# Performance work log

Hardware: AMD Instinct MI355X
Metric: run time of the kernel (lower is better)

Reference implementation:

```python
import jax, jax.numpy as jnp
import numpy as np

NUM_HEADS = 16

def setup_inputs() -> dict:
    key = jax.random.key(0)
    ks = jax.random.split(key, 5)
    B, N, C = 2, 2048, 1024
    x = jax.random.normal(ks[0], (B, N, C), dtype=jnp.float32)
    s_in = 1.0 / np.sqrt(C)
    Wq = jax.random.normal(ks[1], (C, 2 * C), dtype=jnp.float32) * s_in
    Wk = jax.random.normal(ks[2], (C, 2 * C), dtype=jnp.float32) * s_in
    Wv = jax.random.normal(ks[3], (C, 2 * C), dtype=jnp.float32) * s_in
    Wo = jax.random.normal(ks[4], (2 * C, C), dtype=jnp.float32) * (1.0 / np.sqrt(2 * C))
    return {"x": x, "Wq": Wq, "Wk": Wk, "Wv": Wv, "Wo": Wo}

def reference(x, Wq, Wk, Wv, Wo):
    B, N, C = x.shape
    H = NUM_HEADS
    hd = C // H  # head_dim
    def proj(W):
        # [B,N,2C] -> [B,H,N,2*hd]
        return (x @ W).reshape(B, N, H, 2 * hd).transpose(0, 2, 1, 3)
    q = proj(Wq)
    k = proj(Wk)
    v = proj(Wv)
    q_r, q_i = q[..., :hd], q[..., hd:]
    k_r, k_i = k[..., :hd], k[..., hd:]
    v_r, v_i = v[..., :hd], v[..., hd:]
    # complex inner product real part: Re(Q K^H) = q_r.k_r + q_i.k_i
    scores = (jnp.einsum('bhnd,bhmd->bhnm', q_r, k_r)
              + jnp.einsum('bhnd,bhmd->bhnm', q_i, k_i)) / jnp.sqrt(jnp.float32(hd))
    causal = jnp.tril(jnp.ones((N, N), dtype=bool))  # [N,N]
    scores = jnp.where(causal[None, None], scores, -jnp.inf)
    probs = jax.nn.softmax(scores, axis=-1)  # dropout off (eval mode)
    out_r = jnp.einsum('bhnm,bhmd->bhnd', probs, v_r)
    out_i = jnp.einsum('bhnm,bhmd->bhnd', probs, v_i)
    out = jnp.concatenate([out_r, out_i], axis=-1)  # [B,H,N,2*hd]
    out = out.transpose(0, 2, 1, 3).reshape(B, N, 2 * C)
    return out @ Wo  # [B,N,C]
```

## Files before the change

### kernel.cpp

```cpp
#include <hip/hip_runtime.h>
#include <hip/hip_bf16.h>
#include <stdint.h>
#include <cmath>

using bf16 = __hip_bfloat16;
typedef __attribute__((ext_vector_type(8))) short bf16x8;
typedef __attribute__((ext_vector_type(4))) short bf16x4;
typedef __attribute__((ext_vector_type(4))) float f32x4;

#define MFMA16(a, b, c) __builtin_amdgcn_mfma_f32_16x16x32_bf16(a, b, c, 0, 0, 0)

#if defined(__has_builtin)
#if __has_builtin(__builtin_amdgcn_mfma_f32_16x16x16bf16_1k)
#define HAVE_MFMA_K16 1
#endif
#if __has_builtin(__builtin_amdgcn_exp2f)
#define EXP2F __builtin_amdgcn_exp2f
#endif
#endif
#ifndef HAVE_MFMA_K16
#define HAVE_MFMA_K16 0
#endif
#ifndef EXP2F
#define EXP2F exp2f
#endif

#define NEG_BIG (-1e30f)
#define K2SCALE 0.18033688011112042f

__device__ __forceinline__ short f2bf(float v) {
  return __builtin_bit_cast(short, __float2bfloat16(v));
}

__device__ __forceinline__ f32x4 pv_mfma(bf16x4 va, bf16x4 pb, f32x4 c) {
#if HAVE_MFMA_K16
  return __builtin_amdgcn_mfma_f32_16x16x16bf16_1k(va, pb, c, 0, 0, 0);
#else
  const bf16x8 a = {va[0], va[1], va[2], va[3], 0, 0, 0, 0};
  const bf16x8 b = {pb[0], pb[1], pb[2], pb[3], 0, 0, 0, 0};
  return MFMA16(a, b, c);
#endif
}

__device__ __forceinline__ void async_ld16(const bf16* g, bf16* l) {
  __builtin_amdgcn_global_load_lds(
      (const __attribute__((address_space(1))) unsigned int*)g,
      (__attribute__((address_space(3))) unsigned int*)l, 16, 0, 0);
}

template <typename T> __device__ __forceinline__ T cvt_out(float v);
template <> __device__ __forceinline__ float cvt_out<float>(float v) { return v; }
template <> __device__ __forceinline__ bf16 cvt_out<bf16>(float v) { return __float2bfloat16(v); }

__global__ void prep(const float* __restrict__ x,
                     const float* __restrict__ Wq, const float* __restrict__ Wk,
                     const float* __restrict__ Wv, const float* __restrict__ Wo,
                     bf16* __restrict__ xb, bf16* __restrict__ tq,
                     bf16* __restrict__ tk, bf16* __restrict__ tv,
                     bf16* __restrict__ to_) {
  __shared__ bf16 tile[32][33];
  const int bid = blockIdx.x;
  if (bid < 8192) {
    const int z = bid >> 11, tt = bid & 2047;
    const float* in = z == 0 ? Wq : z == 1 ? Wk : z == 2 ? Wv : Wo;
    bf16* out = z == 0 ? tq : z == 1 ? tk : z == 2 ? tv : to_;
    int R, Cc, c0, r0;
    if (z < 3) { R = 1024; Cc = 2048; c0 = (tt & 63) * 32; r0 = (tt >> 6) * 32; }
    else       { R = 2048; Cc = 1024; c0 = (tt & 31) * 32; r0 = (tt >> 5) * 32; }
    const int xx = threadIdx.x & 31;
    const int y = threadIdx.x >> 5;
#pragma unroll
    for (int yy = y; yy < 32; yy += 8)
      tile[yy][xx] = __float2bfloat16(in[(size_t)(r0 + yy) * Cc + c0 + xx]);
    __syncthreads();
#pragma unroll
    for (int yy = y; yy < 32; yy += 8)
      out[(size_t)(c0 + yy) * R + r0 + xx] = tile[xx][yy];
  } else {
    const int i = (bid - 8192) * 256 + threadIdx.x;
    const float4 v = ((const float4*)x)[i];
    bf16 o[4] = {__float2bfloat16(v.x), __float2bfloat16(v.y),
                 __float2bfloat16(v.z), __float2bfloat16(v.w)};
    *(uint64_t*)&xb[i * 4] = *(const uint64_t*)o;
  }
}

__global__ __launch_bounds__(256)
void gemm_qkv(const bf16* __restrict__ xb, const bf16* __restrict__ wq,
              const bf16* __restrict__ wk, const bf16* __restrict__ wv,
              bf16* __restrict__ qo, bf16* __restrict__ ko, bf16* __restrict__ vo) {
  __shared__ __align__(16) bf16 As[128 * 32];
  __shared__ __align__(16) bf16 Bs[128 * 32];
  const int op = blockIdx.y;
  const int bid = blockIdx.x;
  const bf16 *A, *B;
  int m0, n0;
  if (op < 2) { A = xb; B = op ? wk : wq; m0 = (bid >> 4) * 128; n0 = (bid & 15) * 128; }
  else        { A = wv; B = xb;           m0 = (bid & 15) * 128; n0 = (bid >> 4) * 128; }
  const int K = 1024;

  const int t = threadIdx.x;
  const int l = t & 63, w = t >> 6;
  const int q4 = l >> 4, li = l & 15;
  const int wr = (w >> 1) * 64, wc = (w & 1) * 64;

  f32x4 acc[4][4] = {};
  const int colst = (t & 3) * 8;
  const bf16* gA = A + (size_t)m0 * K;
  const bf16* gB = B + (size_t)n0 * K;

  for (int k0 = 0; k0 < K; k0 += 32) {
#pragma unroll
    for (int p = 0; p < 2; ++p) {
      const int row = p * 64 + (t >> 2);
      const int lbase = p * 2048 + (t & ~63) * 8;
      async_ld16(gA + (size_t)row * K + k0 + colst, &As[lbase]);
      async_ld16(gB + (size_t)row * K + k0 + colst, &Bs[lbase]);
    }
    __syncthreads();
    bf16x8 af[4], bfr[4];
#pragma unroll
    for (int i = 0; i < 4; ++i)
      af[i] = *(const bf16x8*)&As[(wr + i * 16 + li) * 32 + q4 * 8];
#pragma unroll
    for (int j = 0; j < 4; ++j)
      bfr[j] = *(const bf16x8*)&Bs[(wc + j * 16 + li) * 32 + q4 * 8];
#pragma unroll
    for (int i = 0; i < 4; ++i)
#pragma unroll
      for (int j = 0; j < 4; ++j)
        acc[i][j] = MFMA16(af[i], bfr[j], acc[i][j]);
    __syncthreads();
  }

#pragma unroll
  for (int i = 0; i < 4; ++i)
#pragma unroll
    for (int j = 0; j < 4; ++j)
#pragma unroll
      for (int r = 0; r < 4; ++r) {
        const int gm = m0 + wr + i * 16 + q4 * 4 + r;
        const int gn = n0 + wc + j * 16 + li;
        const bf16 v = __float2bfloat16(acc[i][j][r]);
        if (op < 2) {
          const int b = gm >> 11, nn = gm & 2047;
          const int h = gn >> 7, d = gn & 127;
          (op ? ko : qo)[((size_t)(b * 16 + h) * 2048 + nn) * 128 + d] = v;
        } else {
          const int h = gm >> 7, d = gm & 127;
          const int b = gn >> 11, nn = gn & 2047;
          vo[((size_t)(b * 16 + h) * 128 + d) * 2048 + nn] = v;
        }
      }
}

template <int NT, typename OT>
__global__ __launch_bounds__(256)
void gemm_bt(const bf16* __restrict__ A, const bf16* __restrict__ B,
             OT* __restrict__ C, int M, int N, int K) {
  __shared__ __align__(16) bf16 As[128 * 32];
  __shared__ __align__(16) bf16 Bs[NT * 32];
  constexpr int JN = NT / 32;
  const int t = threadIdx.x;
  const int l = t & 63, w = t >> 6;
  const int q4 = l >> 4, li = l & 15;
  const int m0 = blockIdx.y * 128;
  const int n0 = blockIdx.x * NT;
  const int wr = (w >> 1) * 64, wc = (w & 1) * (NT / 2);

  f32x4 acc[4][JN] = {};
  const int colst = (t & 3) * 8;
  const bf16* gA = A + (size_t)m0 * K;
  const bf16* gB = B + (size_t)n0 * K;

  for (int k0 = 0; k0 < K; k0 += 32) {
#pragma unroll
    for (int p = 0; p < 2; ++p) {
      const int row = p * 64 + (t >> 2);
      const int lbase = p * 2048 + (t & ~63) * 8;
      async_ld16(gA + (size_t)row * K + k0 + colst, &As[lbase]);
    }
#pragma unroll
    for (int p = 0; p < NT / 64; ++p) {
      const int row = p * 64 + (t >> 2);
      const int lbase = p * 2048 + (t & ~63) * 8;
      async_ld16(gB + (size_t)row * K + k0 + colst, &Bs[lbase]);
    }
    __syncthreads();
    bf16x8 af[4], bfr[JN];
#pragma unroll
    for (int i = 0; i < 4; ++i)
      af[i] = *(const bf16x8*)&As[(wr + i * 16 + li) * 32 + q4 * 8];
#pragma unroll
    for (int j = 0; j < JN; ++j)
      bfr[j] = *(const bf16x8*)&Bs[(wc + j * 16 + li) * 32 + q4 * 8];
#pragma unroll
    for (int i = 0; i < 4; ++i)
#pragma unroll
      for (int j = 0; j < JN; ++j)
        acc[i][j] = MFMA16(af[i], bfr[j], acc[i][j]);
    __syncthreads();
  }

#pragma unroll
  for (int i = 0; i < 4; ++i)
#pragma unroll
    for (int j = 0; j < JN; ++j)
#pragma unroll
      for (int r = 0; r < 4; ++r) {
        const int gm = m0 + wr + i * 16 + q4 * 4 + r;
        const int gn = n0 + wc + j * 16 + li;
        C[(size_t)gm * N + gn] = cvt_out<OT>(acc[i][j][r]);
      }
}

__global__ __launch_bounds__(256, 2)
void flash_attn(const bf16* __restrict__ qm, const bf16* __restrict__ km,
                const bf16* __restrict__ vtm, bf16* __restrict__ om) {
  __shared__ __align__(16) bf16 Ks[64 * 128];
  __shared__ __align__(16) bf16 Vts[128 * 64];

  const int t = threadIdx.x;
  const int l = t & 63, w = t >> 6;
  const int q4 = l >> 4, li = l & 15;
  const int bh = blockIdx.x;
  const int y = blockIdx.y;
  const int qt = (y < 16) ? 31 - y : y - 16;
  const int qs = qt * 64;
  const size_t qkbase = (size_t)bh * 2048 * 128;
  const size_t vbase = (size_t)bh * 128 * 2048;
  const int b = bh >> 4, h = bh & 15;

  bf16x8 qf[4];
  {
    const bf16* Qb = qm + qkbase + (size_t)(qs + w * 16 + li) * 128;
#pragma unroll
    for (int f = 0; f < 4; ++f)
      qf[f] = *(const bf16x8*)(Qb + f * 32 + q4 * 8);
  }

  f32x4 O[8] = {};
  float mrun = NEG_BIG, lrun = 0.f;
  const int gmq = qs + w * 16 + li;

  const int ksrow = t >> 4;
  const int kchu = t & 15;
  const int vsrow = t >> 3;
  const int vchu = t & 7;
  const int wavebase = (t & ~63) * 8;

  const int nt = qt + 1;

  for (int j = 0; j < nt; ++j) {
    const int kb = j * 64;
#pragma unroll
    for (int p = 0; p < 4; ++p) {
      const int kr = p * 16 + ksrow;
      async_ld16(km + qkbase + (size_t)(kb + kr) * 128 + (size_t)((kchu ^ (kr & 7)) * 8),
                 &Ks[p * 2048 + wavebase]);
      const int vr = p * 32 + vsrow;
      async_ld16(vtm + vbase + (size_t)vr * 2048 + kb + (size_t)((vchu ^ (vr & 7)) * 8),
                 &Vts[p * 2048 + wavebase]);
    }
    __syncthreads();

    const bool msk = (j == qt);

    f32x4 S[4];
#pragma unroll
    for (int jk = 0; jk < 4; ++jk) {
      const int krow = jk * 16 + li;
      bf16x8 kf[4];
#pragma unroll
      for (int f = 0; f < 4; ++f)
        kf[f] = *(const bf16x8*)&Ks[krow * 128 + (((f * 4 + q4) ^ (li & 7)) * 8)];
      f32x4 s = {0.f, 0.f, 0.f, 0.f};
#pragma unroll
      for (int f = 0; f < 4; ++f) s = MFMA16(kf[f], qf[f], s);
      S[jk] = s;
    }

    if (msk) {
#pragma unroll
      for (int jk = 0; jk < 4; ++jk)
#pragma unroll
        for (int r = 0; r < 4; ++r)
          if ((kb + jk * 16 + q4 * 4 + r) > gmq) S[jk][r] = NEG_BIG;
    }

    float mx = NEG_BIG;
#pragma unroll
    for (int jk = 0; jk < 4; ++jk)
      mx = fmaxf(mx, fmaxf(fmaxf(S[jk][0], S[jk][1]), fmaxf(S[jk][2], S[jk][3])));
    mx = fmaxf(mx, __shfl_xor(mx, 16));
    mx = fmaxf(mx, __shfl_xor(mx, 32));
    const float mold = mrun;
    const float nm = fmaxf(mrun, mx);
    const bool nomove = (mx <= mold);
    mrun = nm;
    const float nmk = nm * K2SCALE;

    bf16x4 pb[4];
    float rs = 0.f;
#pragma unroll
    for (int jk = 0; jk < 4; ++jk) {
      float e[4];
#pragma unroll
      for (int r = 0; r < 4; ++r) {
        e[r] = EXP2F(__builtin_fmaf(S[jk][r], K2SCALE, -nmk));
        pb[jk][r] = f2bf(e[r]);
      }
      rs += (e[0] + e[1]) + (e[2] + e[3]);
    }
    rs += __shfl_xor(rs, 16);
    rs += __shfl_xor(rs, 32);

    if (__all(nomove)) {
      lrun += rs;
    } else {
      const float alpha = EXP2F((mold - nm) * K2SCALE);
      lrun = lrun * alpha + rs;
#pragma unroll
      for (int dt = 0; dt < 8; ++dt) O[dt] *= alpha;
    }

#pragma unroll
    for (int dt = 0; dt < 8; ++dt)
#pragma unroll
      for (int kc = 0; kc < 4; ++kc) {
        const int gc = kc * 2 + (q4 >> 1);
        const bf16x4 va = *(const bf16x4*)&Vts[(dt * 16 + li) * 64 +
                                               ((gc ^ (li & 7)) * 8) +
                                               (q4 & 1) * 4];
        O[dt] = pv_mfma(va, pb[kc], O[dt]);
      }
    __syncthreads();
  }

  {
    const float inv = 1.0f / lrun;
    const size_t orow = (size_t)(b * 2048 + qs + w * 16 + li) * 2048 + h * 128;
#pragma unroll
    for (int dt = 0; dt < 8; ++dt) {
      bf16x4 o4;
#pragma unroll
      for (int r = 0; r < 4; ++r) o4[r] = f2bf(O[dt][r] * inv);
      *(bf16x4*)&om[orow + dt * 16 + q4 * 4] = o4;
    }
  }
}

extern "C" void kernel_launch(void* const* d_in, const int* in_sizes, int n_in,
                              void* d_out, int out_size, void* d_ws, size_t ws_size,
                              hipStream_t stream) {
  const float* x = (const float*)d_in[0];
  const float* Wq = (const float*)d_in[1];
  const float* Wk = (const float*)d_in[2];
  const float* Wv = (const float*)d_in[3];
  const float* Wo = (const float*)d_in[4];
  float* out = (float*)d_out;

  bf16* ws = (bf16*)d_ws;
  const size_t MEG = 1u << 20;
  bf16* xb = ws;
  bf16* wTq = ws + 4 * MEG;
  bf16* wTk = ws + 6 * MEG;
  bf16* wTv = ws + 8 * MEG;
  bf16* woT = ws + 10 * MEG;
  bf16* at_ws = ws + 2 * MEG;
  bf16* q_ws = ws + 12 * MEG;
  bf16* k_ws = ws + 20 * MEG;
  bf16* vt_ws = ws + 28 * MEG;

  const dim3 blk(256);

  prep<<<dim3(12288), blk, 0, stream>>>(x, Wq, Wk, Wv, Wo, xb, wTq, wTk, wTv, woT);
  gemm_qkv<<<dim3(512, 3), blk, 0, stream>>>(xb, wTq, wTk, wTv, q_ws, k_ws, vt_ws);
  flash_attn<<<dim3(32, 32), blk, 0, stream>>>(q_ws, k_ws, vt_ws, at_ws);
  gemm_bt<64, float><<<dim3(16, 32), blk, 0, stream>>>(at_ws, woT, out, 4096, 1024, 2048);
}
```

Before: 268.6 us.

## Split attention KV tile across two wave groups and merge softmax states

The flash attention block grows from 256 to 512 threads. Each pair of waves shares a 16-row query slice and takes half of the 64-key tile, and waves whose key half lies entirely above the causal diagonal skip it. At the end the two partial softmax states (max, sum, O) are merged through shared memory before the output is written. This doubles the waves available to hide MFMA and LDS latency per tile, at the cost of more registers per block, a multi-stage merge with extra barriers, and idle half-waves on diagonal tiles.

```diff
diff --git a/kernel.cpp b/kernel.cpp
--- a/kernel.cpp
+++ b/kernel.cpp
@@ -214,7 +214,7 @@
       }
 }
 
-__global__ __launch_bounds__(256, 2)
+__global__ __launch_bounds__(512, 2)
 void flash_attn(const bf16* __restrict__ qm, const bf16* __restrict__ km,
                 const bf16* __restrict__ vtm, bf16* __restrict__ om) {
   __shared__ __align__(16) bf16 Ks[64 * 128];
@@ -222,6 +222,7 @@
 
   const int t = threadIdx.x;
   const int l = t & 63, w = t >> 6;
+  const int qg = w & 3, kh = w >> 2;
   const int q4 = l >> 4, li = l & 15;
   const int bh = blockIdx.x;
   const int y = blockIdx.y;
@@ -233,7 +234,7 @@
 
   bf16x8 qf[4];
   {
-    const bf16* Qb = qm + qkbase + (size_t)(qs + w * 16 + li) * 128;
+    const bf16* Qb = qm + qkbase + (size_t)(qs + qg * 16 + li) * 128;
 #pragma unroll
     for (int f = 0; f < 4; ++f)
       qf[f] = *(const bf16x8*)(Qb + f * 32 + q4 * 8);
@@ -241,105 +242,143 @@
 
   f32x4 O[8] = {};
   float mrun = NEG_BIG, lrun = 0.f;
-  const int gmq = qs + w * 16 + li;
+  const int gmq = qs + qg * 16 + li;
+  const int gmqmax = qs + qg * 16 + 15;
+  const int kh32 = kh * 32;
 
   const int ksrow = t >> 4;
   const int kchu = t & 15;
   const int vsrow = t >> 3;
   const int vchu = t & 7;
-  const int wavebase = (t & ~63) * 8;
+  const int dstbase = (t & ~63) * 8;
 
   const int nt = qt + 1;
 
   for (int j = 0; j < nt; ++j) {
     const int kb = j * 64;
 #pragma unroll
-    for (int p = 0; p < 4; ++p) {
-      const int kr = p * 16 + ksrow;
+    for (int p = 0; p < 2; ++p) {
+      const int kr = p * 32 + ksrow;
       async_ld16(km + qkbase + (size_t)(kb + kr) * 128 + (size_t)((kchu ^ (kr & 7)) * 8),
-                 &Ks[p * 2048 + wavebase]);
-      const int vr = p * 32 + vsrow;
+                 &Ks[p * 4096 + dstbase]);
+      const int vr = p * 64 + vsrow;
       async_ld16(vtm + vbase + (size_t)vr * 2048 + kb + (size_t)((vchu ^ (vr & 7)) * 8),
-                 &Vts[p * 2048 + wavebase]);
-    }
-    __syncthreads();
-
-    const bool msk = (j == qt);
-
-    f32x4 S[4];
-#pragma unroll
-    for (int jk = 0; jk < 4; ++jk) {
-      const int krow = jk * 16 + li;
-      bf16x8 kf[4];
-#pragma unroll
-      for (int f = 0; f < 4; ++f)
-        kf[f] = *(const bf16x8*)&Ks[krow * 128 + (((f * 4 + q4) ^ (li & 7)) * 8)];
-      f32x4 s = {0.f, 0.f, 0.f, 0.f};
-#pragma unroll
-      for (int f = 0; f < 4; ++f) s = MFMA16(kf[f], qf[f], s);
-      S[jk] = s;
-    }
-
-    if (msk) {
-#pragma unroll
-      for (int jk = 0; jk < 4; ++jk)
-#pragma unroll
-        for (int r = 0; r < 4; ++r)
-          if ((kb + jk * 16 + q4 * 4 + r) > gmq) S[jk][r] = NEG_BIG;
-    }
-
-    float mx = NEG_BIG;
-#pragma unroll
-    for (int jk = 0; jk < 4; ++jk)
-      mx = fmaxf(mx, fmaxf(fmaxf(S[jk][0], S[jk][1]), fmaxf(S[jk][2], S[jk][3])));
-    mx = fmaxf(mx, __shfl_xor(mx, 16));
-    mx = fmaxf(mx, __shfl_xor(mx, 32));
-    const float mold = mrun;
-    const float nm = fmaxf(mrun, mx);
-    const bool nomove = (mx <= mold);
-    mrun = nm;
-    const float nmk = nm * K2SCALE;
-
-    bf16x4 pb[4];
-    float rs = 0.f;
-#pragma unroll
-    for (int jk = 0; jk < 4; ++jk) {
-      float e[4];
-#pragma unroll
-      for (int r = 0; r < 4; ++r) {
-        e[r] = EXP2F(__builtin_fmaf(S[jk][r], K2SCALE, -nmk));
-        pb[jk][r] = f2bf(e[r]);
-      }
-      rs += (e[0] + e[1]) + (e[2] + e[3]);
-    }
-    rs += __shfl_xor(rs, 16);
-    rs += __shfl_xor(rs, 32);
-
-    if (__all(nomove)) {
-      lrun += rs;
-    } else {
-      const float alpha = EXP2F((mold - nm) * K2SCALE);
-      lrun = lrun * alpha + rs;
-#pragma unroll
-      for (int dt = 0; dt < 8; ++dt) O[dt] *= alpha;
-    }
-
-#pragma unroll
-    for (int dt = 0; dt < 8; ++dt)
-#pragma unroll
-      for (int kc = 0; kc < 4; ++kc) {
-        const int gc = kc * 2 + (q4 >> 1);
-        const bf16x4 va = *(const bf16x4*)&Vts[(dt * 16 + li) * 64 +
-                                               ((gc ^ (li & 7)) * 8) +
-                                               (q4 & 1) * 4];
-        O[dt] = pv_mfma(va, pb[kc], O[dt]);
-      }
-    __syncthreads();
-  }
-
-  {
+                 &Vts[p * 4096 + dstbase]);
+    }
+    __syncthreads();
+
+    if (kb + kh32 <= gmqmax) {
+      const bool msk = (j == qt);
+
+      f32x4 S[2];
+#pragma unroll
+      for (int kc = 0; kc < 2; ++kc) {
+        const int krow = kh32 + kc * 16 + li;
+        bf16x8 kf[4];
+#pragma unroll
+        for (int f = 0; f < 4; ++f)
+          kf[f] = *(const bf16x8*)&Ks[krow * 128 + (((f * 4 + q4) ^ (li & 7)) * 8)];
+        f32x4 s = {0.f, 0.f, 0.f, 0.f};
+#pragma unroll
+        for (int f = 0; f < 4; ++f) s = MFMA16(kf[f], qf[f], s);
+        S[kc] = s;
+      }
+
+      if (msk) {
+#pragma unroll
+        for (int kc = 0; kc < 2; ++kc)
+#pragma unroll
+          for (int r = 0; r < 4; ++r)
+            if ((kb + kh32 + kc * 16 + q4 * 4 + r) > gmq) S[kc][r] = NEG_BIG;
+      }
+
+      float mx = fmaxf(fmaxf(fmaxf(S[0][0], S[0][1]), fmaxf(S[0][2], S[0][3])),
+                       fmaxf(fmaxf(S[1][0], S[1][1]), fmaxf(S[1][2], S[1][3])));
+      mx = fmaxf(mx, __shfl_xor(mx, 16));
+      mx = fmaxf(mx, __shfl_xor(mx, 32));
+      const float mold = mrun;
+      const float nm = fmaxf(mrun, mx);
+      const bool nomove = (mx <= mold);
+      mrun = nm;
+      const float nmk = nm * K2SCALE;
+
+      bf16x4 pb[2];
+      float rs = 0.f;
+#pragma unroll
+      for (int kc = 0; kc < 2; ++kc) {
+        float e[4];
+#pragma unroll
+        for (int r = 0; r < 4; ++r) {
+          e[r] = EXP2F(__builtin_fmaf(S[kc][r], K2SCALE, -nmk));
+          pb[kc][r] = f2bf(e[r]);
+        }
+        rs += (e[0] + e[1]) + (e[2] + e[3]);
+      }
+      rs += __shfl_xor(rs, 16);
+      rs += __shfl_xor(rs, 32);
+
+      if (__all(nomove)) {
+        lrun += rs;
+      } else {
+        const float alpha = EXP2F((mold - nm) * K2SCALE);
+        lrun = lrun * alpha + rs;
+#pragma unroll
+        for (int dt = 0; dt < 8; ++dt) O[dt] *= alpha;
+      }
+
+#pragma unroll
+      for (int dt = 0; dt < 8; ++dt)
+#pragma unroll
+        for (int kc = 0; kc < 2; ++kc) {
+          const int gc = kh * 4 + kc * 2 + (q4 >> 1);
+          const bf16x4 va = *(const bf16x4*)&Vts[(dt * 16 + li) * 64 +
+                                                 ((gc ^ (li & 7)) * 8) +
+                                                 (q4 & 1) * 4];
+          O[dt] = pv_mfma(va, pb[kc], O[dt]);
+        }
+    }
+    __syncthreads();
+  }
+
+  float* mex = (float*)Vts;
+  float* lex = (float*)Vts + 512;
+  float* oex = (float*)Ks;
+  const int idx = qg * 64 + l;
+
+  mex[kh * 256 + idx] = mrun;
+  __syncthreads();
+  const float mo = mex[(kh ^ 1) * 256 + idx];
+  const float ms = fmaxf(mrun, mo);
+  const float al = EXP2F((mrun - ms) * K2SCALE);
+
+  if (kh) {
+    lex[idx] = al * lrun;
+#pragma unroll
+    for (int dt = 0; dt < 4; ++dt) *(f32x4*)&oex[idx * 16 + dt * 4] = O[dt] * al;
+  }
+  __syncthreads();
+  if (!kh) {
+    lrun = al * lrun + lex[idx];
+#pragma unroll
+    for (int dt = 0; dt < 4; ++dt) {
+      const f32x4 o1 = *(const f32x4*)&oex[idx * 16 + dt * 4];
+      O[dt] = O[dt] * al + o1;
+    }
+  }
+  __syncthreads();
+  if (kh) {
+#pragma unroll
+    for (int dt = 0; dt < 4; ++dt) *(f32x4*)&oex[idx * 16 + dt * 4] = O[dt + 4] * al;
+  }
+  __syncthreads();
+  if (!kh) {
+#pragma unroll
+    for (int dt = 0; dt < 4; ++dt) {
+      const f32x4 o1 = *(const f32x4*)&oex[idx * 16 + dt * 4];
+      O[dt + 4] = O[dt + 4] * al + o1;
+    }
     const float inv = 1.0f / lrun;
-    const size_t orow = (size_t)(b * 2048 + qs + w * 16 + li) * 2048 + h * 128;
+    const size_t orow = (size_t)(b * 2048 + qs + qg * 16 + li) * 2048 + h * 128;
 #pragma unroll
     for (int dt = 0; dt < 8; ++dt) {
       bf16x4 o4;
@@ -376,6 +415,6 @@
 
   prep<<<dim3(12288), blk, 0, stream>>>(x, Wq, Wk, Wv, Wo, xb, wTq, wTk, wTv, woT);
   gemm_qkv<<<dim3(512, 3), blk, 0, stream>>>(xb, wTq, wTk, wTv, q_ws, k_ws, vt_ws);
-  flash_attn<<<dim3(32, 32), blk, 0, stream>>>(q_ws, k_ws, vt_ws, at_ws);
+  flash_attn<<<dim3(32, 32), dim3(512), 0, stream>>>(q_ws, k_ws, vt_ws, at_ws);
   gemm_bt<64, float><<<dim3(16, 32), blk, 0, stream>>>(at_ws, woT, out, 4096, 1024, 2048);
 }
```

After: 287.7 us. +7.1%, slower.
